# Kernel tuning notes

Measured on AMD Instinct MI355X. Metric: run time of the kernel, lower is better.

Reference implementation:

```python
import jax, jax.numpy as jnp
import numpy as np

LEAK = 0.2  # tf.nn.leaky_relu default alpha

def leaky(x):
    return jnp.where(x >= 0, x, LEAK * x)

def dense(x, W, b):
    return leaky(x @ W + b)

def lstm_seq(x, Wk, Wr, b):
    # Keras LSTM, gate order [i, f, c, o]; recurrent_activation=sigmoid,
    # activation=leaky_relu (applied to candidate and to c for h).
    B, T, _ = x.shape
    H = Wr.shape[0]
    zx = jnp.einsum('btd,dh->bth', x, Wk) + b  # precompute input projections
    def step(carry, z_t):
        h, c = carry
        z = z_t + h @ Wr
        i, f, g, o = jnp.split(z, 4, axis=-1)
        c = jax.nn.sigmoid(f) * c + jax.nn.sigmoid(i) * leaky(g)
        h = jax.nn.sigmoid(o) * leaky(c)
        return (h, c), h
    init = (jnp.zeros((B, H), x.dtype), jnp.zeros((B, H), x.dtype))
    _, hs = jax.lax.scan(step, init, jnp.swapaxes(zx, 0, 1))  # [T,B,H]
    return jnp.swapaxes(hs, 0, 1)  # [B,T,H]

def setup_inputs() -> dict:
    key = jax.random.key(0)
    ks = iter(jax.random.split(key, 32))
    B, T, F, H = 32, 4096, 11, 128
    data = jax.random.uniform(next(ks), (B, T, F), dtype=jnp.float32)
    def p(i, o):
        W = jax.random.normal(next(ks), (i, o), jnp.float32) * (1.0 / np.sqrt(i))
        return W, jnp.zeros((o,), jnp.float32)
    W_M1, b_M1 = p(6, 8);   W_M2, b_M2 = p(8, 16)
    W_T1, b_T1 = p(11, 8);  W_T2, b_T2 = p(8, 16)
    W_S1, b_S1 = p(58, 32); W_S2, b_S2 = p(32, 64)
    Wk, _ = p(124, 4 * H); Wr, _ = p(H, 4 * H)
    b_l = jnp.zeros((4 * H,), jnp.float32)
    W_P1, b_P1 = p(H, 64); W_P2, b_P2 = p(64, 32)
    W_P3, b_P3 = p(32, 16); W_P4, b_P4 = p(16, 8); W_P5, b_P5 = p(8, 3)
    return dict(data=data, W_M1=W_M1, b_M1=b_M1, W_M2=W_M2, b_M2=b_M2,
                W_T1=W_T1, b_T1=b_T1, W_T2=W_T2, b_T2=b_T2,
                W_S1=W_S1, b_S1=b_S1, W_S2=W_S2, b_S2=b_S2,
                Wk=Wk, Wr=Wr, b_l=b_l,
                W_P1=W_P1, b_P1=b_P1, W_P2=W_P2, b_P2=b_P2,
                W_P3=W_P3, b_P3=b_P3, W_P4=W_P4, b_P4=b_P4,
                W_P5=W_P5, b_P5=b_P5)

def reference(data, W_M1, b_M1, W_M2, b_M2, W_T1, b_T1, W_T2, b_T2,
              W_S1, b_S1, W_S2, b_S2, Wk, Wr, b_l,
              W_P1, b_P1, W_P2, b_P2, W_P3, b_P3, W_P4, b_P4, W_P5, b_P5):
    body = data[:, :, 4:10]
    env = data[:, :, 1:4]
    Ta = data[:, :, 1:2]
    Pa = jnp.log1p(Ta)
    # M tower (dropout is identity at inference)
    M = dense(dense(body, W_M1, b_M1), W_M2, b_M2)
    # Tsk tower with abs
    Tsk = jnp.abs(dense(data, W_T1, b_T1))
    Tsk = jnp.abs(dense(Tsk, W_T2, b_T2))
    Psk = jnp.log1p(Tsk)
    # per-sample concat loops == batched concat on last axis
    s_in = jnp.concatenate([M, Tsk, Psk, Pa, env, body], axis=-1)  # [B,T,58]
    S = dense(dense(s_in, W_S1, b_S1), W_S2, b_S2)  # [B,T,64]
    lstm_in = jnp.concatenate([M, Tsk, Psk, Pa, S, data], axis=-1)  # [B,T,124]
    h = lstm_seq(lstm_in, Wk, Wr, b_l)  # [B,T,128]
    d = dense(h, W_P1, b_P1)
    d = dense(d, W_P2, b_P2)
    d = dense(d, W_P3, b_P3)
    d = dense(d, W_P4, b_P4)
    d = dense(d, W_P5, b_P5)
    out = jax.nn.softmax(d, axis=-1)
    output = out[:, 2:3, :]  # [B,1,3]
    x = jnp.concatenate([data[:, 2:3, 1:], output], axis=-1).reshape(32, 1, 13)
    return (output, x)
```

## Files before the change

### kernel.cpp

```cpp
#include <hip/hip_runtime.h>
#include <math.h>

#define LEAK 0.2f

__device__ __forceinline__ float leaky_f(float x) { return x >= 0.0f ? x : LEAK * x; }
__device__ __forceinline__ float sigmoid_f(float x) { return 1.0f / (1.0f + expf(-x)); }

#define OP1 0
#define OP2 8192
#define OP3 10240
#define OP4 10752
#define OP5 10880
#define OB1 10904
#define OB2 10968
#define OB3 11000
#define OB4 11016
#define OBL 11024
#define OB5 11536
#define WLS_N 11540

__global__ __launch_bounds__(512)
void lstm_cls_kernel(const float* __restrict__ data,
                     const float* __restrict__ W_M1, const float* __restrict__ b_M1,
                     const float* __restrict__ W_M2, const float* __restrict__ b_M2,
                     const float* __restrict__ W_T1, const float* __restrict__ b_T1,
                     const float* __restrict__ W_T2, const float* __restrict__ b_T2,
                     const float* __restrict__ W_S1, const float* __restrict__ b_S1,
                     const float* __restrict__ W_S2, const float* __restrict__ b_S2,
                     const float* __restrict__ Wk,   const float* __restrict__ b_l,
                     const float* __restrict__ Wr,
                     const float* __restrict__ W_P1, const float* __restrict__ b_P1,
                     const float* __restrict__ W_P2, const float* __restrict__ b_P2,
                     const float* __restrict__ W_P3, const float* __restrict__ b_P3,
                     const float* __restrict__ W_P4, const float* __restrict__ b_P4,
                     const float* __restrict__ W_P5, const float* __restrict__ b_P5,
                     float* __restrict__ out)
{
    __shared__ float sdata[3][11];
    __shared__ float feat[3][124];
    __shared__ float m1s[3][8];
    __shared__ float t1s[3][8];
    __shared__ float s1s[3][32];
    __shared__ float dpart[8][3][32];
    __shared__ float epart[4][3][64];
    __shared__ float zpart[4][3][512];
    __shared__ float zx[3][512];
    __shared__ float h[128];
    __shared__ float pp[8][64];
    __shared__ float d1[64], d2[32], d3[16], d4[8], smx[3];
    __shared__ float wls[WLS_N];

    const int b   = blockIdx.x;
    const int tid = threadIdx.x;
    const int q   = tid >> 7;
    const int c4  = tid & 127;
    const float* db = data + (size_t)b * 4096 * 11;

    if (tid < 33) {
        int t = tid / 11, k = tid % 11;
        float v = db[t * 11 + k];
        sdata[t][k] = v;
        feat[t][113 + k] = v;
    }

    const float4* Wr4 = (const float4*)Wr;
    float4 rw[32];
    #pragma unroll
    for (int kk = 0; kk < 32; ++kk)
        rw[kk] = Wr4[(32 * q + kk) * 128 + c4];

    float wB[11]; float bBv = 0.0f;
    float wC[8];  float bCv = 0.0f;
    float bs1v = 0.0f, bs2v = 0.0f;
    if (tid < 24) {
        int j = tid & 7; bBv = b_M1[j];
        #pragma unroll
        for (int k = 0; k < 6; ++k) wB[k] = W_M1[k * 8 + j];
    } else if (tid < 48) {
        int j = (tid - 24) & 7; bBv = b_T1[j];
        #pragma unroll
        for (int k = 0; k < 11; ++k) wB[k] = W_T1[k * 8 + j];
    }
    if (tid < 48) {
        int j = tid & 15; bCv = b_M2[j];
        #pragma unroll
        for (int k = 0; k < 8; ++k) wC[k] = W_M2[k * 16 + j];
    } else if (tid < 96) {
        int j = (tid - 48) & 15; bCv = b_T2[j];
        #pragma unroll
        for (int k = 0; k < 8; ++k) wC[k] = W_T2[k * 16 + j];
    }
    if (tid < 96)  bs1v = b_S1[tid & 31];
    if (tid < 192) bs2v = b_S2[tid & 63];

    if (tid >= 192) {
        int wi = tid - 192;
        float4* wls4 = (float4*)wls;
        for (int i = wi; i < 2048; i += 320) wls4[OP1/4 + i] = ((const float4*)W_P1)[i];
        for (int i = wi; i < 512;  i += 320) wls4[OP2/4 + i] = ((const float4*)W_P2)[i];
        for (int i = wi; i < 128;  i += 320) wls4[OP3/4 + i] = ((const float4*)W_P3)[i];
        for (int i = wi; i < 32;   i += 320) wls4[OP4/4 + i] = ((const float4*)W_P4)[i];
        for (int i = wi; i < 6;    i += 320) wls4[OP5/4 + i] = ((const float4*)W_P5)[i];
        for (int i = wi; i < 16;   i += 320) wls4[OB1/4 + i] = ((const float4*)b_P1)[i];
        for (int i = wi; i < 8;    i += 320) wls4[OB2/4 + i] = ((const float4*)b_P2)[i];
        for (int i = wi; i < 4;    i += 320) wls4[OB3/4 + i] = ((const float4*)b_P3)[i];
        for (int i = wi; i < 2;    i += 320) wls4[OB4/4 + i] = ((const float4*)b_P4)[i];
        for (int i = wi; i < 128;  i += 320) wls4[OBL/4 + i] = ((const float4*)b_l)[i];
        if (wi < 3) wls[OB5 + wi] = b_P5[wi];
    }
    __syncthreads();

    if (tid < 24) {
        int t = tid / 8, j = tid & 7;
        float acc = bBv;
        #pragma unroll
        for (int k = 0; k < 6; ++k) acc += sdata[t][4 + k] * wB[k];
        m1s[t][j] = leaky_f(acc);
    } else if (tid < 48) {
        int u = tid - 24, t = u / 8, j = u & 7;
        float acc = bBv;
        #pragma unroll
        for (int k = 0; k < 11; ++k) acc += sdata[t][k] * wB[k];
        t1s[t][j] = fabsf(leaky_f(acc));
    } else if (tid < 51) {
        int t = tid - 48;
        feat[t][48] = log1pf(sdata[t][1]);
    }
    __syncthreads();

    if (tid < 48) {
        int t = tid / 16, j = tid & 15;
        float acc = bCv;
        #pragma unroll
        for (int k = 0; k < 8; ++k) acc += m1s[t][k] * wC[k];
        feat[t][j] = leaky_f(acc);
    } else if (tid < 96) {
        int u = tid - 48, t = u / 16, j = u & 15;
        float acc = bCv;
        #pragma unroll
        for (int k = 0; k < 8; ++k) acc += t1s[t][k] * wC[k];
        float v = fabsf(leaky_f(acc));
        feat[t][16 + j] = v;
        feat[t][32 + j] = log1pf(v);
    }
    __syncthreads();

    if (tid < 192) {
        int kk = tid & 7, j4 = (tid >> 3) & 7, t = tid >> 6;
        int k0 = kk * 8, k1 = k0 + 8; if (k1 > 58) k1 = 58;
        const float4* WS1_4 = (const float4*)W_S1;
        float4 a = make_float4(0.f, 0.f, 0.f, 0.f);
        for (int k = k0; k < k1; ++k) {
            float4 w = WS1_4[k * 8 + j4];
            float sv = (k < 49) ? feat[t][k] : sdata[t][k - 48];
            a.x = fmaf(sv, w.x, a.x); a.y = fmaf(sv, w.y, a.y);
            a.z = fmaf(sv, w.z, a.z); a.w = fmaf(sv, w.w, a.w);
        }
        ((float4*)&dpart[kk][t][0])[j4] = a;
    }
    __syncthreads();
    if (tid < 96) {
        int t = tid >> 5, j = tid & 31;
        float acc = bs1v;
        #pragma unroll
        for (int kk = 0; kk < 8; ++kk) acc += dpart[kk][t][j];
        s1s[t][j] = leaky_f(acc);
    }
    __syncthreads();

    if (tid < 192) {
        int kk = tid & 3, j4 = (tid >> 2) & 15, t = tid >> 6;
        const float4* WS2_4 = (const float4*)W_S2;
        float4 a = make_float4(0.f, 0.f, 0.f, 0.f);
        #pragma unroll
        for (int i = 0; i < 8; ++i) {
            int k = 8 * kk + i;
            float4 w = WS2_4[k * 16 + j4];
            float sv = s1s[t][k];
            a.x = fmaf(sv, w.x, a.x); a.y = fmaf(sv, w.y, a.y);
            a.z = fmaf(sv, w.z, a.z); a.w = fmaf(sv, w.w, a.w);
        }
        ((float4*)&epart[kk][t][0])[j4] = a;
    }
    __syncthreads();
    if (tid < 192) {
        int t = tid >> 6, j = tid & 63;
        float acc = bs2v;
        #pragma unroll
        for (int kk = 0; kk < 4; ++kk) acc += epart[kk][t][j];
        feat[t][49 + j] = leaky_f(acc);
    }
    __syncthreads();

    {
        const float4* Wk4 = (const float4*)Wk;
        float4 f0 = make_float4(0.f,0.f,0.f,0.f), f1 = f0, f2 = f0;
        #pragma unroll
        for (int i = 0; i < 31; ++i) {
            int k = 31 * q + i;
            float4 w = Wk4[k * 128 + c4];
            float a = feat[0][k], bb = feat[1][k], cc = feat[2][k];
            f0.x = fmaf(a,  w.x, f0.x); f0.y = fmaf(a,  w.y, f0.y);
            f0.z = fmaf(a,  w.z, f0.z); f0.w = fmaf(a,  w.w, f0.w);
            f1.x = fmaf(bb, w.x, f1.x); f1.y = fmaf(bb, w.y, f1.y);
            f1.z = fmaf(bb, w.z, f1.z); f1.w = fmaf(bb, w.w, f1.w);
            f2.x = fmaf(cc, w.x, f2.x); f2.y = fmaf(cc, w.y, f2.y);
            f2.z = fmaf(cc, w.z, f2.z); f2.w = fmaf(cc, w.w, f2.w);
        }
        ((float4*)&zpart[q][0][0])[c4] = f0;
        ((float4*)&zpart[q][1][0])[c4] = f1;
        ((float4*)&zpart[q][2][0])[c4] = f2;
    }
    __syncthreads();
    #pragma unroll
    for (int t = 0; t < 3; ++t) {
        int col = tid;
        zx[t][col] = wls[OBL + col] + zpart[0][t][col] + zpart[1][t][col]
                   + zpart[2][t][col] + zpart[3][t][col];
    }
    __syncthreads();

    float c = 0.0f;
    if (tid < 128) {
        float zi = zx[0][tid], zf = zx[0][128 + tid];
        float zg = zx[0][256 + tid], zo = zx[0][384 + tid];
        (void)zf;
        c = sigmoid_f(zi) * leaky_f(zg);
        h[tid] = sigmoid_f(zo) * leaky_f(c);
    }
    __syncthreads();
    for (int t = 1; t < 3; ++t) {
        float4 acc = make_float4(0.f, 0.f, 0.f, 0.f);
        #pragma unroll
        for (int kk = 0; kk < 32; ++kk) {
            float hk = h[32 * q + kk];
            acc.x = fmaf(hk, rw[kk].x, acc.x);
            acc.y = fmaf(hk, rw[kk].y, acc.y);
            acc.z = fmaf(hk, rw[kk].z, acc.z);
            acc.w = fmaf(hk, rw[kk].w, acc.w);
        }
        ((float4*)&zpart[q][0][0])[c4] = acc;
        __syncthreads();
        if (tid < 128) {
            int j = tid;
            float zi = zx[t][j]       + zpart[0][0][j]       + zpart[1][0][j]       + zpart[2][0][j]       + zpart[3][0][j];
            float zf = zx[t][128 + j] + zpart[0][0][128 + j] + zpart[1][0][128 + j] + zpart[2][0][128 + j] + zpart[3][0][128 + j];
            float zg = zx[t][256 + j] + zpart[0][0][256 + j] + zpart[1][0][256 + j] + zpart[2][0][256 + j] + zpart[3][0][256 + j];
            float zo = zx[t][384 + j] + zpart[0][0][384 + j] + zpart[1][0][384 + j] + zpart[2][0][384 + j] + zpart[3][0][384 + j];
            c = sigmoid_f(zf) * c + sigmoid_f(zi) * leaky_f(zg);
            h[j] = sigmoid_f(zo) * leaky_f(c);
        }
        __syncthreads();
    }

    {
        int part = tid >> 6, jj = tid & 63;
        float acc = 0.0f;
        #pragma unroll
        for (int i = 0; i < 16; ++i) {
            int k = part * 16 + i;
            acc = fmaf(h[k], wls[OP1 + k * 64 + jj], acc);
        }
        pp[part][jj] = acc;
    }
    __syncthreads();
    if (tid < 64) {
        float acc = wls[OB1 + tid];
        #pragma unroll
        for (int p = 0; p < 8; ++p) acc += pp[p][tid];
        d1[tid] = leaky_f(acc);
    }
    __syncthreads();
    if (tid < 256) {
        int part = tid >> 5, jj = tid & 31;
        float acc = 0.0f;
        #pragma unroll
        for (int i = 0; i < 8; ++i) {
            int k = part * 8 + i;
            acc = fmaf(d1[k], wls[OP2 + k * 32 + jj], acc);
        }
        pp[part][jj] = acc;
    }
    __syncthreads();
    if (tid < 32) {
        float acc = wls[OB2 + tid];
        #pragma unroll
        for (int p = 0; p < 8; ++p) acc += pp[p][tid];
        d2[tid] = leaky_f(acc);
    }
    __syncthreads();
    if (tid < 128) {
        int part = tid >> 4, jj = tid & 15;
        float acc = 0.0f;
        #pragma unroll
        for (int i = 0; i < 4; ++i) {
            int k = part * 4 + i;
            acc = fmaf(d2[k], wls[OP3 + k * 16 + jj], acc);
        }
        pp[part][jj] = acc;
    }
    __syncthreads();
    if (tid < 16) {
        float acc = wls[OB3 + tid];
        #pragma unroll
        for (int p = 0; p < 8; ++p) acc += pp[p][tid];
        d3[tid] = leaky_f(acc);
    }
    __syncthreads();
    if (tid < 8) {
        float acc = wls[OB4 + tid];
        #pragma unroll
        for (int k = 0; k < 16; ++k) acc = fmaf(d3[k], wls[OP4 + k * 8 + tid], acc);
        d4[tid] = leaky_f(acc);
    }
    __syncthreads();
    if (tid == 0) {
        float l[3], mx = -1e30f;
        #pragma unroll
        for (int r = 0; r < 3; ++r) {
            float acc = wls[OB5 + r];
            #pragma unroll
            for (int k = 0; k < 8; ++k) acc = fmaf(d4[k], wls[OP5 + k * 3 + r], acc);
            l[r] = leaky_f(acc);
            mx = fmaxf(mx, l[r]);
        }
        float s = 0.0f;
        #pragma unroll
        for (int r = 0; r < 3; ++r) { l[r] = expf(l[r] - mx); s += l[r]; }
        float inv = 1.0f / s;
        #pragma unroll
        for (int r = 0; r < 3; ++r) smx[r] = l[r] * inv;
    }
    __syncthreads();

    if (tid < 3)  out[b * 3 + tid] = smx[tid];
    if (tid < 13) {
        float v = (tid < 10) ? sdata[2][1 + tid] : smx[tid - 10];
        out[96 + b * 13 + tid] = v;
    }
}

extern "C" void kernel_launch(void* const* d_in, const int* in_sizes, int n_in,
                              void* d_out, int out_size, void* d_ws, size_t ws_size,
                              hipStream_t stream) {
    const float* data = (const float*)d_in[0];
    const float* W_M1 = (const float*)d_in[1];
    const float* b_M1 = (const float*)d_in[2];
    const float* W_M2 = (const float*)d_in[3];
    const float* b_M2 = (const float*)d_in[4];
    const float* W_T1 = (const float*)d_in[5];
    const float* b_T1 = (const float*)d_in[6];
    const float* W_T2 = (const float*)d_in[7];
    const float* b_T2 = (const float*)d_in[8];
    const float* W_S1 = (const float*)d_in[9];
    const float* b_S1 = (const float*)d_in[10];
    const float* W_S2 = (const float*)d_in[11];
    const float* b_S2 = (const float*)d_in[12];
    const float* Wk   = (const float*)d_in[13];
    const float* Wr   = (const float*)d_in[14];
    const float* b_l  = (const float*)d_in[15];
    const float* W_P1 = (const float*)d_in[16];
    const float* b_P1 = (const float*)d_in[17];
    const float* W_P2 = (const float*)d_in[18];
    const float* b_P2 = (const float*)d_in[19];
    const float* W_P3 = (const float*)d_in[20];
    const float* b_P3 = (const float*)d_in[21];
    const float* W_P4 = (const float*)d_in[22];
    const float* b_P4 = (const float*)d_in[23];
    const float* W_P5 = (const float*)d_in[24];
    const float* b_P5 = (const float*)d_in[25];
    float* out = (float*)d_out;

    lstm_cls_kernel<<<dim3(32), dim3(512), 0, stream>>>(
        data, W_M1, b_M1, W_M2, b_M2, W_T1, b_T1, W_T2, b_T2,
        W_S1, b_S1, W_S2, b_S2, Wk, b_l, Wr,
        W_P1, b_P1, W_P2, b_P2, W_P3, b_P3, W_P4, b_P4, W_P5, b_P5,
        out);
}
```

Measured before the change: 123.9 us.

## Run small MLP towers in one wavefront with LDS weights and fewer block barriers

Moves the tiny M/T/S dense layers into a single 64-thread wave that reads weights staged in LDS. Wave-level fences replace several block-wide __syncthreads, and the split-K partial buffers are removed. Wk is now prefetched into registers at kernel start, the Wr register load is deferred until after the input projection, and the t=0 gate computation is fused with the zx reduction to drop one barrier. Doing the S layers serially in one wave adds per-thread work, and holding Wk early raises register pressure.

```diff
diff --git a/kernel.cpp b/kernel.cpp
--- a/kernel.cpp
+++ b/kernel.cpp
@@ -6,18 +6,36 @@
 __device__ __forceinline__ float leaky_f(float x) { return x >= 0.0f ? x : LEAK * x; }
 __device__ __forceinline__ float sigmoid_f(float x) { return 1.0f / (1.0f + expf(-x)); }
 
-#define OP1 0
-#define OP2 8192
-#define OP3 10240
-#define OP4 10752
-#define OP5 10880
-#define OB1 10904
-#define OB2 10968
-#define OB3 11000
-#define OB4 11016
-#define OBL 11024
-#define OB5 11536
-#define WLS_N 11540
+__device__ __forceinline__ void wave_lds_fence() {
+    __builtin_amdgcn_wave_barrier();
+    __threadfence_block();
+    __builtin_amdgcn_wave_barrier();
+}
+
+#define OP1  0
+#define OP2  8192
+#define OP3  10240
+#define OP4  10752
+#define OP5  10880
+#define OB1  10904
+#define OB2  10968
+#define OB3  11000
+#define OB4  11016
+#define OBL  11024
+#define OB5  11536
+#define OS1  11540
+#define OS2  13396
+#define OM1  15444
+#define OT1  15492
+#define OM2  15580
+#define OT2  15708
+#define OBM1 15836
+#define OBT1 15844
+#define OBM2 15852
+#define OBT2 15868
+#define OBS1 15884
+#define OBS2 15916
+#define WLS_N 15980
 
 __global__ __launch_bounds__(512)
 void lstm_cls_kernel(const float* __restrict__ data,
@@ -41,10 +59,8 @@
     __shared__ float m1s[3][8];
     __shared__ float t1s[3][8];
     __shared__ float s1s[3][32];
-    __shared__ float dpart[8][3][32];
-    __shared__ float epart[4][3][64];
     __shared__ float zpart[4][3][512];
-    __shared__ float zx[3][512];
+    __shared__ float zx[2][512];
     __shared__ float h[128];
     __shared__ float pp[8][64];
     __shared__ float d1[64], d2[32], d3[16], d4[8], smx[3];
@@ -56,6 +72,12 @@
     const int c4  = tid & 127;
     const float* db = data + (size_t)b * 4096 * 11;
 
+    const float4* Wk4 = (const float4*)Wk;
+    float4 kw[31];
+    #pragma unroll
+    for (int i = 0; i < 31; ++i)
+        kw[i] = Wk4[(31 * q + i) * 128 + c4];
+
     if (tid < 33) {
         int t = tid / 11, k = tid % 11;
         float v = db[t * 11 + k];
@@ -63,142 +85,107 @@
         feat[t][113 + k] = v;
     }
 
-    const float4* Wr4 = (const float4*)Wr;
-    float4 rw[32];
-    #pragma unroll
-    for (int kk = 0; kk < 32; ++kk)
-        rw[kk] = Wr4[(32 * q + kk) * 128 + c4];
-
-    float wB[11]; float bBv = 0.0f;
-    float wC[8];  float bCv = 0.0f;
-    float bs1v = 0.0f, bs2v = 0.0f;
-    if (tid < 24) {
-        int j = tid & 7; bBv = b_M1[j];
-        #pragma unroll
-        for (int k = 0; k < 6; ++k) wB[k] = W_M1[k * 8 + j];
-    } else if (tid < 48) {
-        int j = (tid - 24) & 7; bBv = b_T1[j];
-        #pragma unroll
-        for (int k = 0; k < 11; ++k) wB[k] = W_T1[k * 8 + j];
-    }
-    if (tid < 48) {
-        int j = tid & 15; bCv = b_M2[j];
-        #pragma unroll
-        for (int k = 0; k < 8; ++k) wC[k] = W_M2[k * 16 + j];
-    } else if (tid < 96) {
-        int j = (tid - 48) & 15; bCv = b_T2[j];
-        #pragma unroll
-        for (int k = 0; k < 8; ++k) wC[k] = W_T2[k * 16 + j];
-    }
-    if (tid < 96)  bs1v = b_S1[tid & 31];
-    if (tid < 192) bs2v = b_S2[tid & 63];
-
     if (tid >= 192) {
         int wi = tid - 192;
         float4* wls4 = (float4*)wls;
-        for (int i = wi; i < 2048; i += 320) wls4[OP1/4 + i] = ((const float4*)W_P1)[i];
-        for (int i = wi; i < 512;  i += 320) wls4[OP2/4 + i] = ((const float4*)W_P2)[i];
-        for (int i = wi; i < 128;  i += 320) wls4[OP3/4 + i] = ((const float4*)W_P3)[i];
-        for (int i = wi; i < 32;   i += 320) wls4[OP4/4 + i] = ((const float4*)W_P4)[i];
-        for (int i = wi; i < 6;    i += 320) wls4[OP5/4 + i] = ((const float4*)W_P5)[i];
-        for (int i = wi; i < 16;   i += 320) wls4[OB1/4 + i] = ((const float4*)b_P1)[i];
-        for (int i = wi; i < 8;    i += 320) wls4[OB2/4 + i] = ((const float4*)b_P2)[i];
-        for (int i = wi; i < 4;    i += 320) wls4[OB3/4 + i] = ((const float4*)b_P3)[i];
-        for (int i = wi; i < 2;    i += 320) wls4[OB4/4 + i] = ((const float4*)b_P4)[i];
-        for (int i = wi; i < 128;  i += 320) wls4[OBL/4 + i] = ((const float4*)b_l)[i];
+        for (int i = wi; i < 2048; i += 320) wls4[OP1/4  + i] = ((const float4*)W_P1)[i];
+        for (int i = wi; i < 512;  i += 320) wls4[OP2/4  + i] = ((const float4*)W_P2)[i];
+        for (int i = wi; i < 128;  i += 320) wls4[OP3/4  + i] = ((const float4*)W_P3)[i];
+        for (int i = wi; i < 32;   i += 320) wls4[OP4/4  + i] = ((const float4*)W_P4)[i];
+        for (int i = wi; i < 6;    i += 320) wls4[OP5/4  + i] = ((const float4*)W_P5)[i];
+        for (int i = wi; i < 16;   i += 320) wls4[OB1/4  + i] = ((const float4*)b_P1)[i];
+        for (int i = wi; i < 8;    i += 320) wls4[OB2/4  + i] = ((const float4*)b_P2)[i];
+        for (int i = wi; i < 4;    i += 320) wls4[OB3/4  + i] = ((const float4*)b_P3)[i];
+        for (int i = wi; i < 2;    i += 320) wls4[OB4/4  + i] = ((const float4*)b_P4)[i];
+        for (int i = wi; i < 128;  i += 320) wls4[OBL/4  + i] = ((const float4*)b_l)[i];
+        for (int i = wi; i < 464;  i += 320) wls4[OS1/4  + i] = ((const float4*)W_S1)[i];
+        for (int i = wi; i < 512;  i += 320) wls4[OS2/4  + i] = ((const float4*)W_S2)[i];
+        for (int i = wi; i < 12;   i += 320) wls4[OM1/4  + i] = ((const float4*)W_M1)[i];
+        for (int i = wi; i < 22;   i += 320) wls4[OT1/4  + i] = ((const float4*)W_T1)[i];
+        for (int i = wi; i < 32;   i += 320) wls4[OM2/4  + i] = ((const float4*)W_M2)[i];
+        for (int i = wi; i < 32;   i += 320) wls4[OT2/4  + i] = ((const float4*)W_T2)[i];
+        for (int i = wi; i < 2;    i += 320) wls4[OBM1/4 + i] = ((const float4*)b_M1)[i];
+        for (int i = wi; i < 2;    i += 320) wls4[OBT1/4 + i] = ((const float4*)b_T1)[i];
+        for (int i = wi; i < 4;    i += 320) wls4[OBM2/4 + i] = ((const float4*)b_M2)[i];
+        for (int i = wi; i < 4;    i += 320) wls4[OBT2/4 + i] = ((const float4*)b_T2)[i];
+        for (int i = wi; i < 8;    i += 320) wls4[OBS1/4 + i] = ((const float4*)b_S1)[i];
+        for (int i = wi; i < 16;   i += 320) wls4[OBS2/4 + i] = ((const float4*)b_S2)[i];
         if (wi < 3) wls[OB5 + wi] = b_P5[wi];
     }
     __syncthreads();
 
-    if (tid < 24) {
-        int t = tid / 8, j = tid & 7;
-        float acc = bBv;
-        #pragma unroll
-        for (int k = 0; k < 6; ++k) acc += sdata[t][4 + k] * wB[k];
-        m1s[t][j] = leaky_f(acc);
-    } else if (tid < 48) {
-        int u = tid - 24, t = u / 8, j = u & 7;
-        float acc = bBv;
-        #pragma unroll
-        for (int k = 0; k < 11; ++k) acc += sdata[t][k] * wB[k];
-        t1s[t][j] = fabsf(leaky_f(acc));
-    } else if (tid < 51) {
-        int t = tid - 48;
-        feat[t][48] = log1pf(sdata[t][1]);
-    }
-    __syncthreads();
-
-    if (tid < 48) {
-        int t = tid / 16, j = tid & 15;
-        float acc = bCv;
-        #pragma unroll
-        for (int k = 0; k < 8; ++k) acc += m1s[t][k] * wC[k];
-        feat[t][j] = leaky_f(acc);
-    } else if (tid < 96) {
-        int u = tid - 48, t = u / 16, j = u & 15;
-        float acc = bCv;
-        #pragma unroll
-        for (int k = 0; k < 8; ++k) acc += t1s[t][k] * wC[k];
-        float v = fabsf(leaky_f(acc));
-        feat[t][16 + j] = v;
-        feat[t][32 + j] = log1pf(v);
-    }
-    __syncthreads();
-
-    if (tid < 192) {
-        int kk = tid & 7, j4 = (tid >> 3) & 7, t = tid >> 6;
-        int k0 = kk * 8, k1 = k0 + 8; if (k1 > 58) k1 = 58;
-        const float4* WS1_4 = (const float4*)W_S1;
-        float4 a = make_float4(0.f, 0.f, 0.f, 0.f);
-        for (int k = k0; k < k1; ++k) {
-            float4 w = WS1_4[k * 8 + j4];
-            float sv = (k < 49) ? feat[t][k] : sdata[t][k - 48];
-            a.x = fmaf(sv, w.x, a.x); a.y = fmaf(sv, w.y, a.y);
-            a.z = fmaf(sv, w.z, a.z); a.w = fmaf(sv, w.w, a.w);
-        }
-        ((float4*)&dpart[kk][t][0])[j4] = a;
-    }
-    __syncthreads();
-    if (tid < 96) {
-        int t = tid >> 5, j = tid & 31;
-        float acc = bs1v;
-        #pragma unroll
-        for (int kk = 0; kk < 8; ++kk) acc += dpart[kk][t][j];
-        s1s[t][j] = leaky_f(acc);
-    }
-    __syncthreads();
-
-    if (tid < 192) {
-        int kk = tid & 3, j4 = (tid >> 2) & 15, t = tid >> 6;
-        const float4* WS2_4 = (const float4*)W_S2;
-        float4 a = make_float4(0.f, 0.f, 0.f, 0.f);
-        #pragma unroll
-        for (int i = 0; i < 8; ++i) {
-            int k = 8 * kk + i;
-            float4 w = WS2_4[k * 16 + j4];
-            float sv = s1s[t][k];
-            a.x = fmaf(sv, w.x, a.x); a.y = fmaf(sv, w.y, a.y);
-            a.z = fmaf(sv, w.z, a.z); a.w = fmaf(sv, w.w, a.w);
-        }
-        ((float4*)&epart[kk][t][0])[j4] = a;
-    }
-    __syncthreads();
-    if (tid < 192) {
-        int t = tid >> 6, j = tid & 63;
-        float acc = bs2v;
-        #pragma unroll
-        for (int kk = 0; kk < 4; ++kk) acc += epart[kk][t][j];
-        feat[t][49 + j] = leaky_f(acc);
+    if (tid < 64) {
+        if (tid < 24) {
+            int t = tid / 8, j = tid & 7;
+            float acc = wls[OBM1 + j];
+            #pragma unroll
+            for (int k = 0; k < 6; ++k) acc = fmaf(sdata[t][4 + k], wls[OM1 + k * 8 + j], acc);
+            m1s[t][j] = leaky_f(acc);
+        } else if (tid < 48) {
+            int u = tid - 24, t = u / 8, j = u & 7;
+            float acc = wls[OBT1 + j];
+            #pragma unroll
+            for (int k = 0; k < 11; ++k) acc = fmaf(sdata[t][k], wls[OT1 + k * 8 + j], acc);
+            t1s[t][j] = fabsf(leaky_f(acc));
+        } else if (tid < 51) {
+            int t = tid - 48;
+            feat[t][48] = log1pf(sdata[t][1]);
+        }
+        wave_lds_fence();
+
+        #pragma unroll
+        for (int r = 0; r < 2; ++r) {
+            int idx = tid + 64 * r;
+            if (idx < 48) {
+                int t = idx / 16, j = idx & 15;
+                float acc = wls[OBM2 + j];
+                #pragma unroll
+                for (int k = 0; k < 8; ++k) acc = fmaf(m1s[t][k], wls[OM2 + k * 16 + j], acc);
+                feat[t][j] = leaky_f(acc);
+            } else if (idx < 96) {
+                int u = idx - 48, t = u / 16, j = u & 15;
+                float acc = wls[OBT2 + j];
+                #pragma unroll
+                for (int k = 0; k < 8; ++k) acc = fmaf(t1s[t][k], wls[OT2 + k * 16 + j], acc);
+                float v = fabsf(leaky_f(acc));
+                feat[t][16 + j] = v;
+                feat[t][32 + j] = log1pf(v);
+            }
+        }
+        wave_lds_fence();
+
+        #pragma unroll
+        for (int r = 0; r < 2; ++r) {
+            int idx = tid + 64 * r;
+            if (idx < 96) {
+                int t = idx >> 5, j = idx & 31;
+                float acc = wls[OBS1 + j];
+                for (int k = 0; k < 49; ++k) acc = fmaf(feat[t][k], wls[OS1 + k * 32 + j], acc);
+                #pragma unroll
+                for (int k = 49; k < 58; ++k) acc = fmaf(sdata[t][k - 48], wls[OS1 + k * 32 + j], acc);
+                s1s[t][j] = leaky_f(acc);
+            }
+        }
+        wave_lds_fence();
+
+        #pragma unroll
+        for (int r = 0; r < 3; ++r) {
+            int idx = tid + 64 * r;
+            int t = idx >> 6, j = idx & 63;
+            float acc = wls[OBS2 + j];
+            #pragma unroll
+            for (int k = 0; k < 32; ++k) acc = fmaf(s1s[t][k], wls[OS2 + k * 64 + j], acc);
+            feat[t][49 + j] = leaky_f(acc);
+        }
     }
     __syncthreads();
 
     {
-        const float4* Wk4 = (const float4*)Wk;
         float4 f0 = make_float4(0.f,0.f,0.f,0.f), f1 = f0, f2 = f0;
         #pragma unroll
         for (int i = 0; i < 31; ++i) {
             int k = 31 * q + i;
-            float4 w = Wk4[k * 128 + c4];
+            float4 w = kw[i];
             float a = feat[0][k], bb = feat[1][k], cc = feat[2][k];
             f0.x = fmaf(a,  w.x, f0.x); f0.y = fmaf(a,  w.y, f0.y);
             f0.z = fmaf(a,  w.z, f0.z); f0.w = fmaf(a,  w.w, f0.w);
@@ -212,24 +199,32 @@
         ((float4*)&zpart[q][2][0])[c4] = f2;
     }
     __syncthreads();
+
+    const float4* Wr4 = (const float4*)Wr;
+    float4 rw[32];
     #pragma unroll
-    for (int t = 0; t < 3; ++t) {
-        int col = tid;
-        zx[t][col] = wls[OBL + col] + zpart[0][t][col] + zpart[1][t][col]
-                   + zpart[2][t][col] + zpart[3][t][col];
-    }
-    __syncthreads();
+    for (int kk = 0; kk < 32; ++kk)
+        rw[kk] = Wr4[(32 * q + kk) * 128 + c4];
 
     float c = 0.0f;
+    #pragma unroll
+    for (int r = 0; r < 2; ++r) {
+        int task = tid + 512 * r;
+        int t = task >> 9, col = task & 511;
+        zx[t][col] = wls[OBL + col] + zpart[0][1 + t][col] + zpart[1][1 + t][col]
+                   + zpart[2][1 + t][col] + zpart[3][1 + t][col];
+    }
     if (tid < 128) {
-        float zi = zx[0][tid], zf = zx[0][128 + tid];
-        float zg = zx[0][256 + tid], zo = zx[0][384 + tid];
-        (void)zf;
+        int j = tid;
+        float zi = wls[OBL + j]       + zpart[0][0][j]       + zpart[1][0][j]       + zpart[2][0][j]       + zpart[3][0][j];
+        float zg = wls[OBL + 256 + j] + zpart[0][0][256 + j] + zpart[1][0][256 + j] + zpart[2][0][256 + j] + zpart[3][0][256 + j];
+        float zo = wls[OBL + 384 + j] + zpart[0][0][384 + j] + zpart[1][0][384 + j] + zpart[2][0][384 + j] + zpart[3][0][384 + j];
         c = sigmoid_f(zi) * leaky_f(zg);
-        h[tid] = sigmoid_f(zo) * leaky_f(c);
-    }
-    __syncthreads();
-    for (int t = 1; t < 3; ++t) {
+        h[j] = sigmoid_f(zo) * leaky_f(c);
+    }
+    __syncthreads();
+
+    for (int t = 0; t < 2; ++t) {
         float4 acc = make_float4(0.f, 0.f, 0.f, 0.f);
         #pragma unroll
         for (int kk = 0; kk < 32; ++kk) {
```

After: 125.0 us. About the same (+0.8%).
